# Kernel tuning notes

Hardware: AMD Instinct MI355X
Metric: run time of the kernel (lower is better)

The kernel has to match this reference:

```python
import jax, jax.numpy as jnp
import numpy as np

N_HEADS = 16

def setup_inputs() -> dict:
    key = jax.random.key(0)
    ks = jax.random.split(key, 5)
    D = 1024
    B, T = 4, 1024
    scale = 1.0 / np.sqrt(D)
    x = jax.random.normal(ks[0], (B, T, D), dtype=jnp.float32)
    Wq = jax.random.normal(ks[1], (D, D), dtype=jnp.float32) * scale
    Wk = jax.random.normal(ks[2], (D, D), dtype=jnp.float32) * scale
    Wv = jax.random.normal(ks[3], (D, D), dtype=jnp.float32) * scale
    Wo = jax.random.normal(ks[4], (D, D), dtype=jnp.float32) * scale
    return {"x": x, "Wq": Wq, "Wk": Wk, "Wv": Wv, "Wo": Wo}


def reference(x, Wq, Wk, Wv, Wo):
    # FLA BasedLinearAttention (mode='chunk', normalize=True, scale=1) with
    # Taylor feature map phi(u) = [1, u/d^{1/4}, (u (x) u)/sqrt(2 d)], so
    # phi(q)·phi(k) = 1 + s + s^2/2 where s = (q·k)/sqrt(d).
    B, T, D = x.shape
    H = N_HEADS
    d = D // H  # head_dim == feature_dim
    # torch Linear: y = x @ W.T (bias=False in FLA proj layers)
    q = (x @ Wq.T).reshape(B, T, H, d).transpose(0, 2, 1, 3)  # b h t d
    k = (x @ Wk.T).reshape(B, T, H, d).transpose(0, 2, 1, 3)
    v = (x @ Wv.T).reshape(B, T, H, d).transpose(0, 2, 1, 3)
    s = jnp.einsum('bhtd,bhsd->bhts', q, k) / jnp.sqrt(jnp.float32(d))
    scores = 1.0 + s + 0.5 * s * s  # always > 0 (= ((s+1)^2+1)/2)
    causal = jnp.tril(jnp.ones((T, T), dtype=bool))
    scores = jnp.where(causal, scores, 0.0)
    num = jnp.einsum('bhts,bhsd->bhtd', scores, v)
    den = jnp.sum(scores, axis=-1, keepdims=True)
    o = num / den  # b h t d
    o = o.transpose(0, 2, 1, 3).reshape(B, T, D)  # b t (h d)
    return o @ Wo.T
```

## Files before the change

### kernel.cpp

```cpp
#include <hip/hip_runtime.h>

typedef unsigned short u16;
typedef __attribute__((ext_vector_type(8))) short bf16x8;
typedef __attribute__((ext_vector_type(8))) unsigned short u16x8;
typedef __attribute__((ext_vector_type(4))) float f32x4;

#define MFMA16(a, b, c) __builtin_amdgcn_mfma_f32_16x16x32_bf16((a), (b), (c), 0, 0, 0)

__device__ __forceinline__ void gll16(const void* g, void* l) {
    __builtin_amdgcn_global_load_lds(
        (const __attribute__((address_space(1))) unsigned int*)g,
        (__attribute__((address_space(3))) unsigned int*)l, 16, 0, 0);
}

__device__ __forceinline__ u16 f2b(float f) {
    unsigned int u = __float_as_uint(f);
    u += 0x7fffu + ((u >> 16) & 1u);
    return (u16)(u >> 16);
}

__device__ __forceinline__ unsigned int pkbf(float a, float b) {
    return (unsigned int)f2b(a) | ((unsigned int)f2b(b) << 16);
}

__global__ __launch_bounds__(256) void cast_all(const float* __restrict__ x,
                                                const float* __restrict__ w0,
                                                const float* __restrict__ w1,
                                                const float* __restrict__ w2,
                                                const float* __restrict__ w3,
                                                u16* __restrict__ xb,
                                                u16* __restrict__ wb) {
    const int bid = blockIdx.x;
    const float* s; u16* d; int off;
    if (bid < 2048) { s = x; d = xb; off = bid; }
    else {
        const int wi = (bid - 2048) >> 9;
        s = (wi == 0) ? w0 : (wi == 1) ? w1 : (wi == 2) ? w2 : w3;
        d = wb + (size_t)wi * 1048576;
        off = (bid - 2048) & 511;
    }
    const int i = (off * 256 + threadIdx.x) * 8;
    float4 a = *(const float4*)(s + i);
    float4 b = *(const float4*)(s + i + 4);
    *(uint4*)(d + i) = make_uint4(pkbf(a.x, a.y), pkbf(a.z, a.w),
                                  pkbf(b.x, b.y), pkbf(b.z, b.w));
}

template <int BM, int BN, int MODE>
__global__ __launch_bounds__(256) void gemm_bt(const u16* __restrict__ A,
                                               const u16* __restrict__ W,
                                               void* __restrict__ Yv,
                                               u16* __restrict__ vT,
                                               int K, int ldY) {
    constexpr int MI = BM / 32, NJ = BN / 32;
    constexpr int ACH = BM / 16;
    constexpr int NPW = (BM + BN) / 64;
    __shared__ u16 As[2][BM * 32];
    __shared__ u16 Bs[2][BN * 32];
    const int t = threadIdx.x, w = t >> 6, lane = t & 63;
    const int quad = lane >> 4, m16 = lane & 15;
    const int wr = (w >> 1) * (BM / 2), wc = (w & 1) * (BN / 2);
    const int row0 = blockIdx.x * BM, col0 = blockIdx.y * BN;
    const int srow = lane >> 2, scol = (lane & 3) * 8;

    auto stage = [&](int buf, int k0) {
#pragma unroll
        for (int cc = 0; cc < NPW; ++cc) {
            const int c = w * NPW + cc;
            if (c < ACH)
                gll16(A + (size_t)(row0 + c * 16 + srow) * K + k0 + scol,
                      &As[buf][c * 512]);
            else
                gll16(W + (size_t)(col0 + (c - ACH) * 16 + srow) * K + k0 + scol,
                      &Bs[buf][(c - ACH) * 512]);
        }
    };

    f32x4 acc[MI][NJ];
#pragma unroll
    for (int i = 0; i < MI; ++i)
#pragma unroll
        for (int j = 0; j < NJ; ++j) acc[i][j] = (f32x4){0.f, 0.f, 0.f, 0.f};

    stage(0, 0);
    for (int k0 = 0; k0 < K; k0 += 32) {
        const int buf = (k0 >> 5) & 1;
        __syncthreads();
        if (k0 + 32 < K) stage(buf ^ 1, k0 + 32);
        bf16x8 af[MI], bf[NJ];
#pragma unroll
        for (int i = 0; i < MI; ++i)
            af[i] = *(const bf16x8*)&As[buf][(wr + i * 16 + m16) * 32 + quad * 8];
#pragma unroll
        for (int j = 0; j < NJ; ++j)
            bf[j] = *(const bf16x8*)&Bs[buf][(wc + j * 16 + m16) * 32 + quad * 8];
#pragma unroll
        for (int i = 0; i < MI; ++i)
#pragma unroll
            for (int j = 0; j < NJ; ++j) acc[i][j] = MFMA16(af[i], bf[j], acc[i][j]);
    }
    if constexpr (MODE == 0) {
#pragma unroll
        for (int i = 0; i < MI; ++i)
#pragma unroll
            for (int j = 0; j < NJ; ++j)
#pragma unroll
                for (int r = 0; r < 4; ++r)
                    ((float*)Yv)[(size_t)(row0 + wr + i * 16 + quad * 4 + r) * ldY +
                                 col0 + wc + j * 16 + m16] = acc[i][j][r];
    } else {
        if (col0 < 2048) {
            u16* qk = (u16*)Yv;
#pragma unroll
            for (int i = 0; i < MI; ++i)
#pragma unroll
                for (int j = 0; j < NJ; ++j)
#pragma unroll
                    for (int r = 0; r < 4; ++r)
                        qk[(size_t)(row0 + wr + i * 16 + quad * 4 + r) * 2048 +
                           col0 + wc + j * 16 + m16] = f2b(acc[i][j][r]);
        } else {
#pragma unroll
            for (int i = 0; i < MI; ++i) {
                const int rbase = row0 + wr + i * 16;
                const int bb = rbase >> 10;
                const int tok0 = (rbase & 1023) + quad * 4;
#pragma unroll
                for (int j = 0; j < NJ; ++j) {
                    const int vTrow = bb * 1024 + (col0 + wc + j * 16 + m16 - 2048);
                    *(uint2*)(vT + (size_t)vTrow * 1024 + tok0) =
                        make_uint2(pkbf(acc[i][j][0], acc[i][j][1]),
                                   pkbf(acc[i][j][2], acc[i][j][3]));
                }
            }
        }
    }
}

__global__ __launch_bounds__(256) void based_attn(const u16* __restrict__ qkm,
                                                  const u16* __restrict__ vT,
                                                  u16* __restrict__ o) {
    __shared__ u16 qsA[2][64][32];
    __shared__ u16 qsB[2][64][32];
    __shared__ u16 ks[2][2][64][32];
    __shared__ u16 vs[2][2][64][32];
    __shared__ u16 SsA[2][64][32];
    __shared__ u16 SsB[2][64][32];

    const int t = threadIdx.x, w = t >> 6, lane = t & 63;
    const int quad = lane >> 4, m16 = lane & 15;
    const int p = blockIdx.x, h = blockIdx.y, b = blockIdx.z;
    const int tA = p, tB = 15 - p;
    const int srow = lane >> 2, s8 = (lane & 3) * 8;

    const size_t qbase = (size_t)b * 1024 * 2048 + h * 64;
    const size_t kbase = qbase + 1024;
    const size_t vbase = ((size_t)b * 1024 + h * 64) * 1024;

#pragma unroll
    for (int cc = 0; cc < 4; ++cc) {
        const int c = w * 4 + cc;
        const int tile = c >> 3, dblk = (c >> 2) & 1, rc = c & 3;
        const int Q0 = (tile ? tB : tA) * 64;
        gll16(qkm + qbase + (size_t)(Q0 + rc * 16 + srow) * 2048 + dblk * 32 + s8,
              tile ? &qsB[dblk][rc * 16][0] : &qsA[dblk][rc * 16][0]);
    }
#pragma unroll
    for (int cc = 0; cc < 2; ++cc) {
        const int c = w * 2 + cc;
        const int blk = c >> 2, rc = c & 3;
        gll16(qkm + kbase + (size_t)(rc * 16 + srow) * 2048 + blk * 32 + s8,
              &ks[0][blk][rc * 16][0]);
        gll16(vT + vbase + (size_t)(rc * 16 + srow) * 1024 + blk * 32 + s8,
              &vs[0][blk][rc * 16][0]);
    }

    bf16x8 ones;
#pragma unroll
    for (int e = 0; e < 8; ++e) ones[e] = (short)0x3F80;

    f32x4 numA[4], numB[4], denA, denB;
    denA = denB = (f32x4){0.f, 0.f, 0.f, 0.f};
#pragma unroll
    for (int j = 0; j < 4; ++j) numA[j] = numB[j] = (f32x4){0.f, 0.f, 0.f, 0.f};

    const int qrow = w * 16 + m16;

    for (int kt = 0; kt <= tB; ++kt) {
        const int buf = kt & 1;
        __syncthreads();
        if (kt < tB) {
            const int nb = buf ^ 1, kn = kt + 1;
#pragma unroll
            for (int cc = 0; cc < 2; ++cc) {
                const int c = w * 2 + cc;
                const int blk = c >> 2, rc = c & 3;
                gll16(qkm + kbase + (size_t)(kn * 64 + rc * 16 + srow) * 2048 + blk * 32 + s8,
                      &ks[nb][blk][rc * 16][0]);
                gll16(vT + vbase + (size_t)(rc * 16 + srow) * 1024 + kn * 64 + blk * 32 + s8,
                      &vs[nb][blk][rc * 16][0]);
            }
        }
        const bool doA = (kt <= tA);

        f32x4 sA[4], sB[4];
#pragma unroll
        for (int jk = 0; jk < 4; ++jk)
            sA[jk] = sB[jk] = (f32x4){0.f, 0.f, 0.f, 0.f};
#pragma unroll
        for (int kd = 0; kd < 2; ++kd) {
            bf16x8 qfB = *(const bf16x8*)&qsB[kd][qrow][quad * 8];
            bf16x8 qfA = *(const bf16x8*)&qsA[kd][qrow][quad * 8];
#pragma unroll
            for (int jk = 0; jk < 4; ++jk) {
                bf16x8 af = *(const bf16x8*)&ks[buf][kd][jk * 16 + m16][quad * 8];
                sB[jk] = MFMA16(af, qfB, sB[jk]);
                if (doA) sA[jk] = MFMA16(af, qfA, sA[jk]);
            }
        }
#pragma unroll
        for (int jk = 0; jk < 4; ++jk) {
            const int key0 = jk * 16 + quad * 4;
            const int kl = jk * 16 + quad * 4;
            float scB[4];
#pragma unroll
            for (int r = 0; r < 4; ++r) {
                const float u = fmaf(sB[jk][r], 0.125f, 1.0f);
                scB[r] = fmaf(u * 0.5f, u, 0.5f);
            }
            if (kt == tB) {
#pragma unroll
                for (int r = 0; r < 4; ++r)
                    if (key0 + r > qrow) scB[r] = 0.f;
            }
            *(uint2*)&SsB[kl >> 5][qrow][kl & 31] =
                make_uint2(pkbf(scB[0], scB[1]), pkbf(scB[2], scB[3]));
            if (doA) {
                float scA[4];
#pragma unroll
                for (int r = 0; r < 4; ++r) {
                    const float u = fmaf(sA[jk][r], 0.125f, 1.0f);
                    scA[r] = fmaf(u * 0.5f, u, 0.5f);
                }
                if (kt == tA) {
#pragma unroll
                    for (int r = 0; r < 4; ++r)
                        if (key0 + r > qrow) scA[r] = 0.f;
                }
                *(uint2*)&SsA[kl >> 5][qrow][kl & 31] =
                    make_uint2(pkbf(scA[0], scA[1]), pkbf(scA[2], scA[3]));
            }
        }
#pragma unroll
        for (int kb = 0; kb < 2; ++kb) {
            bf16x8 vf[4];
#pragma unroll
            for (int j = 0; j < 4; ++j)
                vf[j] = *(const bf16x8*)&vs[buf][kb][j * 16 + m16][quad * 8];
            bf16x8 sfB = *(const bf16x8*)&SsB[kb][qrow][quad * 8];
#pragma unroll
            for (int j = 0; j < 4; ++j) numB[j] = MFMA16(sfB, vf[j], numB[j]);
            denB = MFMA16(sfB, ones, denB);
            if (doA) {
                bf16x8 sfA = *(const bf16x8*)&SsA[kb][qrow][quad * 8];
#pragma unroll
                for (int j = 0; j < 4; ++j) numA[j] = MFMA16(sfA, vf[j], numA[j]);
                denA = MFMA16(sfA, ones, denA);
            }
        }
    }

#pragma unroll
    for (int r = 0; r < 4; ++r) {
        const float invA = 1.0f / denA[r], invB = 1.0f / denB[r];
        const int rowoff = w * 16 + quad * 4 + r;
        const size_t tokA = (size_t)(b * 1024 + tA * 64 + rowoff);
        const size_t tokB = (size_t)(b * 1024 + tB * 64 + rowoff);
#pragma unroll
        for (int j = 0; j < 4; ++j) {
            o[tokA * 1024 + h * 64 + j * 16 + m16] = f2b(numA[j][r] * invA);
            o[tokB * 1024 + h * 64 + j * 16 + m16] = f2b(numB[j][r] * invB);
        }
    }
}

extern "C" void kernel_launch(void* const* d_in, const int* in_sizes, int n_in,
                              void* d_out, int out_size, void* d_ws, size_t ws_size,
                              hipStream_t stream) {
    const float* x  = (const float*)d_in[0];
    const float* Wq = (const float*)d_in[1];
    const float* Wk = (const float*)d_in[2];
    const float* Wv = (const float*)d_in[3];
    const float* Wo = (const float*)d_in[4];
    float* out = (float*)d_out;

    const size_t MEL = 4096ull * 1024ull;
    u16* xb   = (u16*)d_ws;
    u16* Wqkv = xb + MEL;
    u16* Wob  = Wqkv + 3ull * 1024 * 1024;
    u16* qk   = Wob + 1024ull * 1024;
    u16* vT   = qk + 2ull * MEL;
    u16* o    = vT + MEL;

    cast_all<<<4096, 256, 0, stream>>>(x, Wq, Wk, Wv, Wo, xb, Wqkv);

    dim3 gq(32, 24);
    gemm_bt<128, 128, 1><<<gq, 256, 0, stream>>>(xb, Wqkv, qk, vT, 1024, 2048);

    dim3 ga(8, 16, 4);
    based_attn<<<ga, 256, 0, stream>>>(qk, vT, o);

    dim3 go(64, 16);
    gemm_bt<64, 64, 0><<<go, 256, 0, stream>>>(o, Wob, (void*)out, nullptr, 1024, 1024);
}
```

Before: 166.7 us.

## Load K/V and Q fragments directly into registers with register double-buffering

Replaces the LDS staging of Q, K and V tiles (global_load_lds plus block-wide barriers) with direct per-lane global loads into MFMA fragment registers. K/V fragments are double-buffered in registers across iterations, and the loop-level __syncthreads is removed. This frees LDS and sets occupancy to 2 blocks per CU via launch bounds. The cost is that each wave redundantly loads the full K/V tiles from global/L2, since all 4 waves need the same tiles. It also adds register pressure and drops any barrier protecting the score scratch buffers SsA/SsB.

```diff
diff --git a/kernel.cpp b/kernel.cpp
--- a/kernel.cpp
+++ b/kernel.cpp
@@ -137,13 +137,11 @@
     }
 }
 
-__global__ __launch_bounds__(256) void based_attn(const u16* __restrict__ qkm,
-                                                  const u16* __restrict__ vT,
-                                                  u16* __restrict__ o) {
-    __shared__ u16 qsA[2][64][32];
-    __shared__ u16 qsB[2][64][32];
-    __shared__ u16 ks[2][2][64][32];
-    __shared__ u16 vs[2][2][64][32];
+struct KVFrags { bf16x8 k[2][4]; bf16x8 v[2][4]; };
+
+__global__ __launch_bounds__(256, 2) void based_attn(const u16* __restrict__ qkm,
+                                                     const u16* __restrict__ vT,
+                                                     u16* __restrict__ o) {
     __shared__ u16 SsA[2][64][32];
     __shared__ u16 SsB[2][64][32];
 
@@ -151,28 +149,19 @@
     const int quad = lane >> 4, m16 = lane & 15;
     const int p = blockIdx.x, h = blockIdx.y, b = blockIdx.z;
     const int tA = p, tB = 15 - p;
-    const int srow = lane >> 2, s8 = (lane & 3) * 8;
+    const int qrow = w * 16 + m16;
 
     const size_t qbase = (size_t)b * 1024 * 2048 + h * 64;
     const size_t kbase = qbase + 1024;
     const size_t vbase = ((size_t)b * 1024 + h * 64) * 1024;
 
-#pragma unroll
-    for (int cc = 0; cc < 4; ++cc) {
-        const int c = w * 4 + cc;
-        const int tile = c >> 3, dblk = (c >> 2) & 1, rc = c & 3;
-        const int Q0 = (tile ? tB : tA) * 64;
-        gll16(qkm + qbase + (size_t)(Q0 + rc * 16 + srow) * 2048 + dblk * 32 + s8,
-              tile ? &qsB[dblk][rc * 16][0] : &qsA[dblk][rc * 16][0]);
-    }
-#pragma unroll
-    for (int cc = 0; cc < 2; ++cc) {
-        const int c = w * 2 + cc;
-        const int blk = c >> 2, rc = c & 3;
-        gll16(qkm + kbase + (size_t)(rc * 16 + srow) * 2048 + blk * 32 + s8,
-              &ks[0][blk][rc * 16][0]);
-        gll16(vT + vbase + (size_t)(rc * 16 + srow) * 1024 + blk * 32 + s8,
-              &vs[0][blk][rc * 16][0]);
+    bf16x8 qfA[2], qfB[2];
+#pragma unroll
+    for (int kd = 0; kd < 2; ++kd) {
+        qfA[kd] = *(const bf16x8*)(qkm + qbase +
+                   (size_t)(tA * 64 + qrow) * 2048 + kd * 32 + quad * 8);
+        qfB[kd] = *(const bf16x8*)(qkm + qbase +
+                   (size_t)(tB * 64 + qrow) * 2048 + kd * 32 + quad * 8);
     }
 
     bf16x8 ones;
@@ -184,43 +173,36 @@
 #pragma unroll
     for (int j = 0; j < 4; ++j) numA[j] = numB[j] = (f32x4){0.f, 0.f, 0.f, 0.f};
 
-    const int qrow = w * 16 + m16;
-
-    for (int kt = 0; kt <= tB; ++kt) {
-        const int buf = kt & 1;
-        __syncthreads();
-        if (kt < tB) {
-            const int nb = buf ^ 1, kn = kt + 1;
-#pragma unroll
-            for (int cc = 0; cc < 2; ++cc) {
-                const int c = w * 2 + cc;
-                const int blk = c >> 2, rc = c & 3;
-                gll16(qkm + kbase + (size_t)(kn * 64 + rc * 16 + srow) * 2048 + blk * 32 + s8,
-                      &ks[nb][blk][rc * 16][0]);
-                gll16(vT + vbase + (size_t)(rc * 16 + srow) * 1024 + kn * 64 + blk * 32 + s8,
-                      &vs[nb][blk][rc * 16][0]);
-            }
-        }
+    auto load_tile = [&](int kt, KVFrags& F) {
+#pragma unroll
+        for (int kd = 0; kd < 2; ++kd)
+#pragma unroll
+            for (int jk = 0; jk < 4; ++jk)
+                F.k[kd][jk] = *(const bf16x8*)(qkm + kbase +
+                    (size_t)(kt * 64 + jk * 16 + m16) * 2048 + kd * 32 + quad * 8);
+#pragma unroll
+        for (int kb = 0; kb < 2; ++kb)
+#pragma unroll
+            for (int j = 0; j < 4; ++j)
+                F.v[kb][j] = *(const bf16x8*)(vT + vbase +
+                    (size_t)(j * 16 + m16) * 1024 + kt * 64 + kb * 32 + quad * 8);
+    };
+
+    auto compute = [&](const KVFrags& F, int kt) {
         const bool doA = (kt <= tA);
-
         f32x4 sA[4], sB[4];
 #pragma unroll
         for (int jk = 0; jk < 4; ++jk)
             sA[jk] = sB[jk] = (f32x4){0.f, 0.f, 0.f, 0.f};
 #pragma unroll
-        for (int kd = 0; kd < 2; ++kd) {
-            bf16x8 qfB = *(const bf16x8*)&qsB[kd][qrow][quad * 8];
-            bf16x8 qfA = *(const bf16x8*)&qsA[kd][qrow][quad * 8];
+        for (int kd = 0; kd < 2; ++kd)
 #pragma unroll
             for (int jk = 0; jk < 4; ++jk) {
-                bf16x8 af = *(const bf16x8*)&ks[buf][kd][jk * 16 + m16][quad * 8];
-                sB[jk] = MFMA16(af, qfB, sB[jk]);
-                if (doA) sA[jk] = MFMA16(af, qfA, sA[jk]);
-            }
-        }
+                sB[jk] = MFMA16(F.k[kd][jk], qfB[kd], sB[jk]);
+                if (doA) sA[jk] = MFMA16(F.k[kd][jk], qfA[kd], sA[jk]);
+            }
 #pragma unroll
         for (int jk = 0; jk < 4; ++jk) {
-            const int key0 = jk * 16 + quad * 4;
             const int kl = jk * 16 + quad * 4;
             float scB[4];
 #pragma unroll
@@ -231,7 +213,7 @@
             if (kt == tB) {
 #pragma unroll
                 for (int r = 0; r < 4; ++r)
-                    if (key0 + r > qrow) scB[r] = 0.f;
+                    if (kl + r > qrow) scB[r] = 0.f;
             }
             *(uint2*)&SsB[kl >> 5][qrow][kl & 31] =
                 make_uint2(pkbf(scB[0], scB[1]), pkbf(scB[2], scB[3]));
@@ -245,7 +227,7 @@
                 if (kt == tA) {
 #pragma unroll
                     for (int r = 0; r < 4; ++r)
-                        if (key0 + r > qrow) scA[r] = 0.f;
+                        if (kl + r > qrow) scA[r] = 0.f;
                 }
                 *(uint2*)&SsA[kl >> 5][qrow][kl & 31] =
                     make_uint2(pkbf(scA[0], scA[1]), pkbf(scA[2], scA[3]));
@@ -253,21 +235,29 @@
         }
 #pragma unroll
         for (int kb = 0; kb < 2; ++kb) {
-            bf16x8 vf[4];
-#pragma unroll
-            for (int j = 0; j < 4; ++j)
-                vf[j] = *(const bf16x8*)&vs[buf][kb][j * 16 + m16][quad * 8];
             bf16x8 sfB = *(const bf16x8*)&SsB[kb][qrow][quad * 8];
 #pragma unroll
-            for (int j = 0; j < 4; ++j) numB[j] = MFMA16(sfB, vf[j], numB[j]);
+            for (int j = 0; j < 4; ++j) numB[j] = MFMA16(sfB, F.v[kb][j], numB[j]);
             denB = MFMA16(sfB, ones, denB);
             if (doA) {
                 bf16x8 sfA = *(const bf16x8*)&SsA[kb][qrow][quad * 8];
 #pragma unroll
-                for (int j = 0; j < 4; ++j) numA[j] = MFMA16(sfA, vf[j], numA[j]);
+                for (int j = 0; j < 4; ++j) numA[j] = MFMA16(sfA, F.v[kb][j], numA[j]);
                 denA = MFMA16(sfA, ones, denA);
             }
         }
+    };
+
+    KVFrags F0, F1;
+    load_tile(0, F0);
+    int kt = 0;
+    while (true) {
+        if (kt < tB) load_tile(kt + 1, F1);
+        compute(F0, kt);
+        if (++kt > tB) break;
+        if (kt < tB) load_tile(kt + 1, F0);
+        compute(F1, kt);
+        if (++kt > tB) break;
     }
 
 #pragma unroll
```

After: 199.9 us. +20.0%, slower.
